# Optimization experiments

Hardware: AMD Instinct MI355X
Metric: run time of the kernel (lower is better)

The kernel has to match this reference:

```python
import jax, jax.numpy as jnp
import numpy as np

G, N, E = 4, 50000, 400000   # subgraphs, nodes/graph, edges/graph
D = 128                      # num_node_feat = num_g_hid = out_g_ch
L = 3                        # num_layers
NE, AH = 8, 64               # num_expert, num_att_hid
FE = 8                       # num_edge_feat (unused by GIN conv)
LN_EPS = 1e-5


def setup_inputs() -> dict:
    key = jax.random.key(0)
    ks = jax.random.split(key, 12)
    s = 1.0 / np.sqrt(D)
    inp = {
        "decomp_x": jax.random.normal(ks[0], (G, N, D), dtype=jnp.float32),
        "decomp_edge_index": jax.random.randint(ks[1], (G, 2, E), 0, N, dtype=jnp.int32),
        "decomp_edge_attr": jax.random.normal(ks[2], (G, E, FE), dtype=jnp.float32),
        # GIN MLP params per layer: Linear(D,D) -> ReLU -> Linear(D,D), stored [in,out]
        "Ws1": jax.random.uniform(ks[3], (L, D, D), jnp.float32, -s, s),
        "bs1": jax.random.uniform(ks[4], (L, D), jnp.float32, -s, s),
        "Ws2": jax.random.uniform(ks[5], (L, D, D), jnp.float32, -s, s),
        "bs2": jax.random.uniform(ks[6], (L, D), jnp.float32, -s, s),
        "ln_g": jnp.ones((L, D), jnp.float32),
        "ln_b": jnp.zeros((L, D), jnp.float32),
        # Attention: w1 [n_hidden, v_hidden], w2 [n_expert, n_hidden]
        "att_w1": jax.random.uniform(ks[7], (AH, D), jnp.float32, -1.0 / np.sqrt(D), 1.0 / np.sqrt(D)),
        "att_w2": jax.random.uniform(ks[8], (NE, AH), jnp.float32, -1.0 / np.sqrt(AH), 1.0 / np.sqrt(AH)),
    }
    return inp


def _layer_norm(h, g, b):
    mu = jnp.mean(h, axis=-1, keepdims=True)
    var = jnp.var(h, axis=-1, keepdims=True)
    return (h - mu) * jax.lax.rsqrt(var + LN_EPS) * g + b


def _gin_graph(x, edge_index, Ws1, bs1, Ws2, bs2, ln_g, ln_b):
    # x: [N, D]; edge_index: [2, E] (src, dst)
    src, dst = edge_index[0], edge_index[1]
    for l in range(L):
        identity = x
        # GINConv (eps=0): MLP(x_i + sum_{j->i} x_j)
        agg = jax.ops.segment_sum(x[src], dst, num_segments=N)  # gather+scatter
        h = x + agg
        h = jnp.maximum(h @ Ws1[l] + bs1[l], 0.0) @ Ws2[l] + bs2[l]
        if l < L - 1:
            h = h + identity  # same dims, no projection
        x = _layer_norm(h, ln_g[l], ln_b[l])
    return jnp.sum(x, axis=0)  # [D] graph readout (sum over nodes)


def reference(decomp_x, decomp_edge_index, decomp_edge_attr,
              Ws1, bs1, Ws2, bs2, ln_g, ln_b, att_w1, att_w2):
    # edge_attr is unused by the GIN conv path (only NaN-checked in torch)
    g = jax.vmap(_gin_graph, in_axes=(0, 0, None, None, None, None, None, None))(
        decomp_x, decomp_edge_index, Ws1, bs1, Ws2, bs2, ln_g, ln_b)  # [G, D]
    # Attention pooling over subgraph vectors
    support = jnp.tanh(att_w1 @ g.T)                 # [AH, G]
    att = jax.nn.softmax(att_w2 @ support, axis=1)   # [NE, G]
    pooled = att @ g                                 # [NE, D]
    return pooled.reshape(1, NE * D)                 # [1, NE*D]
```

## Files before the change

### kernel.cpp

```cpp
#include <hip/hip_runtime.h>
#include <math.h>

#define G 4
#define NN 50000
#define EE 400000
#define D 128
#define LN_EPS 1e-5f
#define BPG 782

typedef _Float16 f16;
typedef _Float16 f16x4 __attribute__((ext_vector_type(4)));
typedef _Float16 f16x8 __attribute__((ext_vector_type(8)));
typedef float f32x4 __attribute__((ext_vector_type(4)));


__global__ __launch_bounds__(256) void hist_kernel(const int* __restrict__ ei, int* __restrict__ deg) {
    int idx = blockIdx.x * 256 + threadIdx.x;
    if (idx >= G * EE) return;
    int g = idx / EE, e = idx - g * EE;
    int dst = ei[g * 2 * EE + EE + e];
    atomicAdd(&deg[g * NN + dst], 1);
}

__global__ __launch_bounds__(256) void scan_kernel(const int* __restrict__ deg, int* __restrict__ row_start,
                                                   int* __restrict__ cursor) {
    int g = blockIdx.x, t = threadIdx.x;
    const int C = (NN + 255) / 256;
    __shared__ int sums[256];
    int start = t * C, end = min(start + C, NN);
    int s = 0;
    for (int i = start; i < end; ++i) s += deg[g * NN + i];
    sums[t] = s;
    __syncthreads();
    for (int off = 1; off < 256; off <<= 1) {
        int v = (t >= off) ? sums[t - off] : 0;
        __syncthreads();
        sums[t] += v;
        __syncthreads();
    }
    int run = (t == 0) ? 0 : sums[t - 1];
    for (int i = start; i < end; ++i) {
        row_start[g * (NN + 1) + i] = run;
        cursor[g * NN + i] = run;
        run += deg[g * NN + i];
    }
    if (t == 255) row_start[g * (NN + 1) + NN] = sums[255];
}

__global__ __launch_bounds__(256) void place_kernel(const int* __restrict__ ei, int* __restrict__ cursor,
                                                    int* __restrict__ csr_src) {
    int idx = blockIdx.x * 256 + threadIdx.x;
    if (idx >= G * EE) return;
    int g = idx / EE, e = idx - g * EE;
    int src = ei[g * 2 * EE + e];
    int dst = ei[g * 2 * EE + EE + e];
    int pos = atomicAdd(&cursor[g * NN + dst], 1);
    csr_src[g * EE + pos] = src;
}


__global__ __launch_bounds__(256) void cast_x_kernel(const float* __restrict__ x, f16* __restrict__ o) {
    int i = blockIdx.x * 256 + threadIdx.x;
    float4 v = ((const float4*)x)[i];
    f16x4 h = {(f16)v.x, (f16)v.y, (f16)v.z, (f16)v.w};
    ((f16x4*)o)[i] = h;
}

__global__ __launch_bounds__(256) void cast_w_kernel(const float* __restrict__ Ws1, const float* __restrict__ Ws2,
                                                     f16* __restrict__ Wt) {
    int e = blockIdx.x * 256 + threadIdx.x;
    int mat = e >> 14, r = (e >> 7) & 127, c = e & 127;
    const float* src = (mat < 3) ? (Ws1 + mat * 16384) : (Ws2 + (mat - 3) * 16384);
    Wt[e] = (f16)src[c * 128 + r];
}


__global__ __launch_bounds__(256) void gin_layer(
    const f16* __restrict__ Xin, f16* __restrict__ Xout,
    const int* __restrict__ row_start, const int* __restrict__ csr_src,
    const f16* __restrict__ W1t, const f16* __restrict__ W2t,
    const float* __restrict__ b1, const float* __restrict__ b2,
    const float* __restrict__ lng, const float* __restrict__ lnb,
    int has_res, int do_read, float* __restrict__ gvec)
{
    __shared__ f16 A[64][136];
    __shared__ f16 ID[64][136];
    __shared__ f16 WL[128][136];
    __shared__ float colsum[128];

    int t = threadIdx.x;
    int g = blockIdx.x / BPG, bb = blockIdx.x - g * BPG;
    int nrow0 = bb * 64;
    long row0 = (long)g * NN + nrow0;
    int valid = min(64, NN - nrow0);

    if (do_read && t < 128) colsum[t] = 0.f;

    f16x8 wtmp[8];
#pragma unroll
    for (int i = 0; i < 8; ++i)
        wtmp[i] = *(const f16x8*)(W1t + i * 2048 + t * 8);

    {
        int grp = t >> 4, lane = t & 15;
        const int* rs = row_start + g * (NN + 1);
        const int* srcs = csr_src + (long)g * EE;
        long gbase = (long)g * NN * 16;
        const f16x8* Xv = (const f16x8*)Xin;
#pragma unroll
        for (int i = 0; i < 4; ++i) {
            int r = grp * 4 + i;
            if (r < valid) {
                int n = nrow0 + r;
                f16x8 self = Xv[(row0 + r) * 16 + lane];
                if (has_res) *(f16x8*)&ID[r][lane * 8] = self;
                float acc[8];
#pragma unroll
                for (int j = 0; j < 8; ++j) acc[j] = (float)self[j];
                int s0 = rs[n], s1 = rs[n + 1];
                int k = s0;
                for (; k + 1 < s1; k += 2) {
                    f16x8 v0 = Xv[gbase + (long)srcs[k] * 16 + lane];
                    f16x8 v1 = Xv[gbase + (long)srcs[k + 1] * 16 + lane];
#pragma unroll
                    for (int j = 0; j < 8; ++j) acc[j] += (float)v0[j] + (float)v1[j];
                }
                if (k < s1) {
                    f16x8 v0 = Xv[gbase + (long)srcs[k] * 16 + lane];
#pragma unroll
                    for (int j = 0; j < 8; ++j) acc[j] += (float)v0[j];
                }
                f16x8 o;
#pragma unroll
                for (int j = 0; j < 8; ++j) o[j] = (f16)acc[j];
                *(f16x8*)&A[r][lane * 8] = o;
            } else {
                f16x8 z = {0, 0, 0, 0, 0, 0, 0, 0};
                *(f16x8*)&A[r][lane * 8] = z;
            }
        }
    }

    {
        int wr = t >> 4, wc = (t & 15) * 8;
#pragma unroll
        for (int i = 0; i < 8; ++i)
            *(f16x8*)&WL[i * 16 + (t >> 4)][wc] = wtmp[i];
    }
    __syncthreads();

    int w = t >> 6, l = t & 63, q = l >> 4, cl = l & 15;
    int mrow = w * 16 + cl;

    f32x4 acc[8];
#pragma unroll
    for (int ns = 0; ns < 8; ++ns) acc[ns] = (f32x4){0.f, 0.f, 0.f, 0.f};
#pragma unroll
    for (int kc = 0; kc < 4; ++kc) {
        f16x8 a = *(const f16x8*)&A[mrow][kc * 32 + q * 8];
#pragma unroll
        for (int ns = 0; ns < 8; ++ns) {
            f16x8 b = *(const f16x8*)&WL[ns * 16 + cl][kc * 32 + q * 8];
            acc[ns] = __builtin_amdgcn_mfma_f32_16x16x32_f16(a, b, acc[ns], 0, 0, 0);
        }
    }

#pragma unroll
    for (int i = 0; i < 8; ++i)
        wtmp[i] = *(const f16x8*)(W2t + i * 2048 + t * 8);

    __syncthreads();

#pragma unroll
    for (int ns = 0; ns < 8; ++ns) {
        float bv = b1[ns * 16 + cl];
#pragma unroll
        for (int r = 0; r < 4; ++r) {
            float v = fmaxf(acc[ns][r] + bv, 0.f);
            A[w * 16 + q * 4 + r][ns * 16 + cl] = (f16)v;
        }
    }
    {
        int wc = (t & 15) * 8;
#pragma unroll
        for (int i = 0; i < 8; ++i)
            *(f16x8*)&WL[i * 16 + (t >> 4)][wc] = wtmp[i];
    }
    __syncthreads();

    f32x4 acc2[8];
#pragma unroll
    for (int ns = 0; ns < 8; ++ns) acc2[ns] = (f32x4){0.f, 0.f, 0.f, 0.f};
#pragma unroll
    for (int kc = 0; kc < 4; ++kc) {
        f16x8 a = *(const f16x8*)&A[mrow][kc * 32 + q * 8];
#pragma unroll
        for (int ns = 0; ns < 8; ++ns) {
            f16x8 b = *(const f16x8*)&WL[ns * 16 + cl][kc * 32 + q * 8];
            acc2[ns] = __builtin_amdgcn_mfma_f32_16x16x32_f16(a, b, acc2[ns], 0, 0, 0);
        }
    }

    float o[8][4];
    float gm[8], gb[8];
#pragma unroll
    for (int ns = 0; ns < 8; ++ns) {
        int col = ns * 16 + cl;
        float b2v = b2[col];
        gm[ns] = lng[col];
        gb[ns] = lnb[col];
#pragma unroll
        for (int r = 0; r < 4; ++r) o[ns][r] = acc2[ns][r] + b2v;
    }
    if (has_res) {
#pragma unroll
        for (int r = 0; r < 4; ++r) {
            int lr = w * 16 + q * 4 + r;
#pragma unroll
            for (int ns = 0; ns < 8; ++ns) o[ns][r] += (float)ID[lr][ns * 16 + cl];
        }
    }

#pragma unroll
    for (int r = 0; r < 4; ++r) {
        float s1 = 0.f, s2 = 0.f;
#pragma unroll
        for (int ns = 0; ns < 8; ++ns) { s1 += o[ns][r]; s2 += o[ns][r] * o[ns][r]; }
        s1 += __shfl_xor(s1, 1); s2 += __shfl_xor(s2, 1);
        s1 += __shfl_xor(s1, 2); s2 += __shfl_xor(s2, 2);
        s1 += __shfl_xor(s1, 4); s2 += __shfl_xor(s2, 4);
        s1 += __shfl_xor(s1, 8); s2 += __shfl_xor(s2, 8);
        float mean = s1 * (1.f / 128.f);
        float var = s2 * (1.f / 128.f) - mean * mean;
        float rstd = rsqrtf(var + LN_EPS);
#pragma unroll
        for (int ns = 0; ns < 8; ++ns) o[ns][r] = (o[ns][r] - mean) * rstd * gm[ns] + gb[ns];
    }

    if (!do_read) {
#pragma unroll
        for (int ns = 0; ns < 8; ++ns)
#pragma unroll
            for (int r = 0; r < 4; ++r)
                A[w * 16 + q * 4 + r][ns * 16 + cl] = (f16)o[ns][r];
        __syncthreads();
        int row = t >> 2, seg = t & 3;
        if (row < valid) {
            f16* dst = Xout + (row0 + row) * 128 + seg * 32;
            *(f16x8*)(dst) = *(const f16x8*)&A[row][seg * 32];
            *(f16x8*)(dst + 8) = *(const f16x8*)&A[row][seg * 32 + 8];
            *(f16x8*)(dst + 16) = *(const f16x8*)&A[row][seg * 32 + 16];
            *(f16x8*)(dst + 24) = *(const f16x8*)&A[row][seg * 32 + 24];
        }
    } else {
#pragma unroll
        for (int ns = 0; ns < 8; ++ns) {
            float v = 0.f;
#pragma unroll
            for (int r = 0; r < 4; ++r) {
                int lr = w * 16 + q * 4 + r;
                if (lr < valid) v += o[ns][r];
            }
            v += __shfl_xor(v, 16);
            v += __shfl_xor(v, 32);
            if (l < 16) atomicAdd(&colsum[ns * 16 + cl], v);
        }
        __syncthreads();
        if (t < 128) atomicAdd(&gvec[g * 128 + t], colsum[t]);
    }
}


__global__ __launch_bounds__(256) void att_kernel(const float* __restrict__ gvec, const float* __restrict__ w1,
                                                  const float* __restrict__ w2, float* __restrict__ out) {
    __shared__ float sup[64][4];
    __shared__ float att[8][4];
    int t = threadIdx.x;
    int ah = t >> 2, gg = t & 3;
    float d = 0.f;
    for (int k = 0; k < 128; ++k) d += w1[ah * 128 + k] * gvec[gg * 128 + k];
    sup[ah][gg] = tanhf(d);
    __syncthreads();
    if (t < 32) {
        int ne = t >> 2, g2 = t & 3;
        float sc = 0.f;
        for (int k = 0; k < 64; ++k) sc += w2[ne * 64 + k] * sup[k][g2];
        att[ne][g2] = sc;
    }
    __syncthreads();
    if (t < 8) {
        float m = fmaxf(fmaxf(att[t][0], att[t][1]), fmaxf(att[t][2], att[t][3]));
        float e0 = expf(att[t][0] - m), e1 = expf(att[t][1] - m);
        float e2 = expf(att[t][2] - m), e3 = expf(att[t][3] - m);
        float inv = 1.f / (e0 + e1 + e2 + e3);
        att[t][0] = e0 * inv; att[t][1] = e1 * inv; att[t][2] = e2 * inv; att[t][3] = e3 * inv;
    }
    __syncthreads();
    for (int o = t; o < 1024; o += 256) {
        int ne = o >> 7, dd = o & 127;
        float v = 0.f;
        for (int g2 = 0; g2 < 4; ++g2) v += att[ne][g2] * gvec[g2 * 128 + dd];
        out[o] = v;
    }
}


extern "C" void kernel_launch(void* const* d_in, const int* in_sizes, int n_in,
                              void* d_out, int out_size, void* d_ws, size_t ws_size,
                              hipStream_t stream) {
    const float* x   = (const float*)d_in[0];
    const int*   ei  = (const int*)d_in[1];
    const float* Ws1 = (const float*)d_in[3];
    const float* bs1 = (const float*)d_in[4];
    const float* Ws2 = (const float*)d_in[5];
    const float* bs2 = (const float*)d_in[6];
    const float* lng = (const float*)d_in[7];
    const float* lnb = (const float*)d_in[8];
    const float* aw1 = (const float*)d_in[9];
    const float* aw2 = (const float*)d_in[10];

    char* ws = (char*)d_ws;
    f16*   XA       = (f16*)(ws);
    f16*   XB       = (f16*)(ws + 51200000);
    int*   csr_src  = (int*)(ws + 102400000);
    int*   row_start= (int*)(ws + 108800000);
    int*   cursor   = (int*)(ws + 109600256);
    int*   deg      = (int*)(ws + 110400256);
    f16*   Wt       = (f16*)(ws + 111200256);
    float* gvec     = (float*)(ws + 111396864);

    hipMemsetAsync(deg, 0, G * NN * sizeof(int), stream);
    hipMemsetAsync(gvec, 0, G * D * sizeof(float), stream);

    hist_kernel<<<(G * EE + 255) / 256, 256, 0, stream>>>(ei, deg);
    scan_kernel<<<G, 256, 0, stream>>>(deg, row_start, cursor);
    place_kernel<<<(G * EE + 255) / 256, 256, 0, stream>>>(ei, cursor, csr_src);

    cast_x_kernel<<<(G * NN * D / 4) / 256, 256, 0, stream>>>(x, XA);
    cast_w_kernel<<<(6 * D * D) / 256, 256, 0, stream>>>(Ws1, Ws2, Wt);

    f16* Xcur = XA;
    f16* Xnxt = XB;
    for (int l = 0; l < 3; ++l) {
        gin_layer<<<G * BPG, 256, 0, stream>>>(Xcur, Xnxt, row_start, csr_src,
                                               Wt + l * D * D, Wt + (3 + l) * D * D,
                                               bs1 + l * D, bs2 + l * D,
                                               lng + l * D, lnb + l * D,
                                               (l < 2) ? 1 : 0, (l == 2) ? 1 : 0, gvec);
        f16* tmp = Xcur; Xcur = Xnxt; Xnxt = tmp;
    }
    att_kernel<<<1, 256, 0, stream>>>(gvec, aw1, aw2, (float*)d_out);
}
```

Before: 1.024 ms.

## Drop LDS weight staging and block barriers in GIN layer, widen scan

The GIN layer kernel no longer stages the two 128x128 weight matrices in shared memory. Each wave now reads its MFMA B fragments straight from global memory through the caches, and the block-wide barriers are removed because each wave only touches its own 16 rows of A. This cuts shared memory per block roughly in half and adds a launch-bounds occupancy hint, aiming for more resident blocks to hide gather latency. The neighbour gather is unrolled by four to keep more loads in flight, and the CSR scan runs with 1024 threads instead of 256. In exchange, every wave repeats the weight loads from L1/L2 instead of sharing one copy in LDS.

```diff
diff --git a/kernel.cpp b/kernel.cpp
--- a/kernel.cpp
+++ b/kernel.cpp
@@ -22,17 +22,17 @@
     atomicAdd(&deg[g * NN + dst], 1);
 }
 
-__global__ __launch_bounds__(256) void scan_kernel(const int* __restrict__ deg, int* __restrict__ row_start,
-                                                   int* __restrict__ cursor) {
+__global__ __launch_bounds__(1024) void scan_kernel(const int* __restrict__ deg, int* __restrict__ row_start,
+                                                    int* __restrict__ cursor) {
     int g = blockIdx.x, t = threadIdx.x;
-    const int C = (NN + 255) / 256;
-    __shared__ int sums[256];
+    const int C = (NN + 1023) / 1024;
+    __shared__ int sums[1024];
     int start = t * C, end = min(start + C, NN);
     int s = 0;
     for (int i = start; i < end; ++i) s += deg[g * NN + i];
     sums[t] = s;
     __syncthreads();
-    for (int off = 1; off < 256; off <<= 1) {
+    for (int off = 1; off < 1024; off <<= 1) {
         int v = (t >= off) ? sums[t - off] : 0;
         __syncthreads();
         sums[t] += v;
@@ -44,7 +44,7 @@
         cursor[g * NN + i] = run;
         run += deg[g * NN + i];
     }
-    if (t == 255) row_start[g * (NN + 1) + NN] = sums[255];
+    if (t == 1023) row_start[g * (NN + 1) + NN] = sums[1023];
 }
 
 __global__ __launch_bounds__(256) void place_kernel(const int* __restrict__ ei, int* __restrict__ cursor,
@@ -75,7 +75,7 @@
 }
 
 
-__global__ __launch_bounds__(256) void gin_layer(
+__global__ __launch_bounds__(256, 4) void gin_layer(
     const f16* __restrict__ Xin, f16* __restrict__ Xout,
     const int* __restrict__ row_start, const int* __restrict__ csr_src,
     const f16* __restrict__ W1t, const f16* __restrict__ W2t,
@@ -85,7 +85,6 @@
 {
     __shared__ f16 A[64][136];
     __shared__ f16 ID[64][136];
-    __shared__ f16 WL[128][136];
     __shared__ float colsum[128];
 
     int t = threadIdx.x;
@@ -94,12 +93,10 @@
     long row0 = (long)g * NN + nrow0;
     int valid = min(64, NN - nrow0);
 
-    if (do_read && t < 128) colsum[t] = 0.f;
-
-    f16x8 wtmp[8];
-#pragma unroll
-    for (int i = 0; i < 8; ++i)
-        wtmp[i] = *(const f16x8*)(W1t + i * 2048 + t * 8);
+    if (do_read) {
+        if (t < 128) colsum[t] = 0.f;
+        __syncthreads();
+    }
 
     {
         int grp = t >> 4, lane = t & 15;
@@ -119,13 +116,16 @@
                 for (int j = 0; j < 8; ++j) acc[j] = (float)self[j];
                 int s0 = rs[n], s1 = rs[n + 1];
                 int k = s0;
-                for (; k + 1 < s1; k += 2) {
+                for (; k + 3 < s1; k += 4) {
                     f16x8 v0 = Xv[gbase + (long)srcs[k] * 16 + lane];
                     f16x8 v1 = Xv[gbase + (long)srcs[k + 1] * 16 + lane];
-#pragma unroll
-                    for (int j = 0; j < 8; ++j) acc[j] += (float)v0[j] + (float)v1[j];
+                    f16x8 v2 = Xv[gbase + (long)srcs[k + 2] * 16 + lane];
+                    f16x8 v3 = Xv[gbase + (long)srcs[k + 3] * 16 + lane];
+#pragma unroll
+                    for (int j = 0; j < 8; ++j)
+                        acc[j] += ((float)v0[j] + (float)v1[j]) + ((float)v2[j] + (float)v3[j]);
                 }
-                if (k < s1) {
+                for (; k < s1; ++k) {
                     f16x8 v0 = Xv[gbase + (long)srcs[k] * 16 + lane];
 #pragma unroll
                     for (int j = 0; j < 8; ++j) acc[j] += (float)v0[j];
@@ -141,17 +141,10 @@
         }
     }
 
-    {
-        int wr = t >> 4, wc = (t & 15) * 8;
-#pragma unroll
-        for (int i = 0; i < 8; ++i)
-            *(f16x8*)&WL[i * 16 + (t >> 4)][wc] = wtmp[i];
-    }
-    __syncthreads();
-
     int w = t >> 6, l = t & 63, q = l >> 4, cl = l & 15;
     int mrow = w * 16 + cl;
 
+    const f16x8* Wb1 = (const f16x8*)W1t + (cl * 16 + q);
     f32x4 acc[8];
 #pragma unroll
     for (int ns = 0; ns < 8; ++ns) acc[ns] = (f32x4){0.f, 0.f, 0.f, 0.f};
@@ -160,16 +153,10 @@
         f16x8 a = *(const f16x8*)&A[mrow][kc * 32 + q * 8];
 #pragma unroll
         for (int ns = 0; ns < 8; ++ns) {
-            f16x8 b = *(const f16x8*)&WL[ns * 16 + cl][kc * 32 + q * 8];
+            f16x8 b = Wb1[ns * 256 + kc * 4];
             acc[ns] = __builtin_amdgcn_mfma_f32_16x16x32_f16(a, b, acc[ns], 0, 0, 0);
         }
     }
-
-#pragma unroll
-    for (int i = 0; i < 8; ++i)
-        wtmp[i] = *(const f16x8*)(W2t + i * 2048 + t * 8);
-
-    __syncthreads();
 
 #pragma unroll
     for (int ns = 0; ns < 8; ++ns) {
@@ -180,14 +167,8 @@
             A[w * 16 + q * 4 + r][ns * 16 + cl] = (f16)v;
         }
     }
-    {
-        int wc = (t & 15) * 8;
-#pragma unroll
-        for (int i = 0; i < 8; ++i)
-            *(f16x8*)&WL[i * 16 + (t >> 4)][wc] = wtmp[i];
-    }
-    __syncthreads();
-
+
+    const f16x8* Wb2 = (const f16x8*)W2t + (cl * 16 + q);
     f32x4 acc2[8];
 #pragma unroll
     for (int ns = 0; ns < 8; ++ns) acc2[ns] = (f32x4){0.f, 0.f, 0.f, 0.f};
@@ -196,7 +177,7 @@
         f16x8 a = *(const f16x8*)&A[mrow][kc * 32 + q * 8];
 #pragma unroll
         for (int ns = 0; ns < 8; ++ns) {
-            f16x8 b = *(const f16x8*)&WL[ns * 16 + cl][kc * 32 + q * 8];
+            f16x8 b = Wb2[ns * 256 + kc * 4];
             acc2[ns] = __builtin_amdgcn_mfma_f32_16x16x32_f16(a, b, acc2[ns], 0, 0, 0);
         }
     }
@@ -243,14 +224,14 @@
 #pragma unroll
             for (int r = 0; r < 4; ++r)
                 A[w * 16 + q * 4 + r][ns * 16 + cl] = (f16)o[ns][r];
-        __syncthreads();
-        int row = t >> 2, seg = t & 3;
-        if (row < valid) {
-            f16* dst = Xout + (row0 + row) * 128 + seg * 32;
-            *(f16x8*)(dst) = *(const f16x8*)&A[row][seg * 32];
-            *(f16x8*)(dst + 8) = *(const f16x8*)&A[row][seg * 32 + 8];
-            *(f16x8*)(dst + 16) = *(const f16x8*)&A[row][seg * 32 + 16];
-            *(f16x8*)(dst + 24) = *(const f16x8*)&A[row][seg * 32 + 24];
+        int rr = w * 16 + (l >> 2), seg = l & 3;
+        if (rr < valid) {
+            f16* dst = Xout + (row0 + rr) * 128 + seg * 32;
+            const f16* srcp = &A[rr][seg * 32];
+            *(f16x8*)(dst)      = *(const f16x8*)(srcp);
+            *(f16x8*)(dst + 8)  = *(const f16x8*)(srcp + 8);
+            *(f16x8*)(dst + 16) = *(const f16x8*)(srcp + 16);
+            *(f16x8*)(dst + 24) = *(const f16x8*)(srcp + 24);
         }
     } else {
 #pragma unroll
@@ -333,7 +314,7 @@
     hipMemsetAsync(gvec, 0, G * D * sizeof(float), stream);
 
     hist_kernel<<<(G * EE + 255) / 256, 256, 0, stream>>>(ei, deg);
-    scan_kernel<<<G, 256, 0, stream>>>(deg, row_start, cursor);
+    scan_kernel<<<G, 1024, 0, stream>>>(deg, row_start, cursor);
     place_kernel<<<(G * EE + 255) / 256, 256, 0, stream>>>(ei, cursor, csr_src);
 
     cast_x_kernel<<<(G * NN * D / 4) / 256, 256, 0, stream>>>(x, XA);
```

Result: faster. 981.2 us (-4.1%).
